# Kernel tuning notes

Measured on AMD Instinct MI355X. Metric: run time of the kernel, lower is better.

## Reference

```python
import jax, jax.numpy as jnp
import numpy as np

B, S, D, H = 4, 1024, 1024, 16
DK = D // H


def _linear_params(key, scale):
    kw, kb = jax.random.split(key)
    W = jax.random.normal(kw, (D, D), dtype=jnp.float32) * scale
    b = jax.random.normal(kb, (D,), dtype=jnp.float32) * 0.01
    return W, b


def setup_inputs() -> dict:
    key = jax.random.key(0)
    ks = jax.random.split(key, 12)
    scale = 1.0 / np.sqrt(D)
    inp = {
        "query": jax.random.normal(ks[0], (B, S, D), dtype=jnp.float32),
        "key": jax.random.normal(ks[1], (B, S, D), dtype=jnp.float32),
        "value": jax.random.normal(ks[2], (B, S, D), dtype=jnp.float32),
        "time_k": jax.random.normal(ks[3], (B, S, D), dtype=jnp.float32),
        "time_v": jax.random.normal(ks[4], (B, S, D), dtype=jnp.float32),
        "mask": jnp.zeros((B, 1, S, S), dtype=jnp.float32),
    }
    names = ["Wq", "bq", "Wk", "bk", "Wv", "bv", "Wtk", "btk", "Wtv", "btv", "Wm", "bm"]
    for i in range(6):
        W, b = _linear_params(ks[5 + i], scale)
        inp[names[2 * i]] = W
        inp[names[2 * i + 1]] = b
    return inp


def _split_heads(x):
    # [B,S,D] -> [B,H,S,DK]
    b, s, _ = x.shape
    return x.reshape(b, s, H, DK).transpose(0, 2, 1, 3)


def reference(query, key, value, time_k, time_v, mask,
              Wq, bq, Wk, bk, Wv, bv, Wtk, btk, Wtv, btv, Wm, bm):
    q = _split_heads(query @ Wq + bq)
    k = _split_heads(key @ Wk + bk)
    v = _split_heads(value @ Wv + bv)
    t_k = _split_heads(time_k @ Wtk + btk)
    t_v = _split_heads(time_v @ Wtv + btv)

    # scores[b,h,i,j] = q_i . k_j + t_k_i . q_j  (note second term uses q on the key axis)
    scores = jnp.einsum("bhid,bhjd->bhij", q, k) + jnp.einsum("bhid,bhjd->bhij", t_k, q)
    # module divides by sqrt(d_model) (query.size(-1)), not sqrt(d_k)
    scores = scores / jnp.sqrt(jnp.float32(D)) + mask
    probs = jax.nn.softmax(scores, axis=-1)

    # dropout is identity (p=0 / eval); squeeze(-2) is a no-op for S>1
    context = jnp.einsum("bhij,bhjd->bhid", probs, v) + jnp.einsum("bhij,bhjd->bhid", probs, t_v)
    x = context.transpose(0, 2, 1, 3).reshape(query.shape[0], -1, D)
    return x @ Wm + bm
```

## Files before the change

kernel.cpp:

```cpp
#include <hip/hip_runtime.h>
#include <hip/hip_bf16.h>
#include <cstdint>
#include <cstddef>

typedef __bf16 bf16;
typedef bf16 bf16x8 __attribute__((ext_vector_type(8)));
typedef bf16 bf16x4 __attribute__((ext_vector_type(4)));
typedef float f32x4 __attribute__((ext_vector_type(4)));
typedef unsigned int u32;

#define DEV static __device__ __forceinline__

DEV f32x4 mfma16(bf16x8 a, bf16x8 b, f32x4 c) {
    return __builtin_amdgcn_mfma_f32_16x16x32_bf16(a, b, c, 0, 0, 0);
}

DEV f32x4 shflx4(f32x4 v, int m) {
    f32x4 r;
    for (int i = 0; i < 4; ++i) r[i] = __shfl_xor(v[i], m, 64);
    return r;
}

DEV bf16x8 cvt8(const float* p) {
    float4 f0 = *(const float4*)p;
    float4 f1 = *(const float4*)(p + 4);
    bf16x8 v;
    v[0] = (bf16)f0.x; v[1] = (bf16)f0.y; v[2] = (bf16)f0.z; v[3] = (bf16)f0.w;
    v[4] = (bf16)f1.x; v[5] = (bf16)f1.y; v[6] = (bf16)f1.z; v[7] = (bf16)f1.w;
    return v;
}

DEV void glo(const bf16* g, bf16* l) {
    __builtin_amdgcn_global_load_lds(
        (const __attribute__((address_space(1))) u32*)g,
        (__attribute__((address_space(3))) u32*)l,
        16, 0, 0);
}

#define WAITB(n) asm volatile("s_waitcnt vmcnt(" #n ")\n\ts_barrier" ::: "memory")
#define BAR()    asm volatile("s_barrier" ::: "memory")

struct PrepArgs {
    const float* w[6];
    const float* act[5];
    const float* mask;
    bf16* wdst[6];  int wstride[6];
    bf16* adst[5];  int astride[5];
    bf16* maskR;
};

__global__ __launch_bounds__(256) void prep_kernel(PrepArgs p)
{
    const int z = blockIdx.z;
    const int t = threadIdx.x;
    if (z < 6) {
        __shared__ bf16 tile[64][72];
        const float* src = p.w[z];
        bf16* out = p.wdst[z];
        const int os = p.wstride[z];
        const int r = t >> 3, c8 = (t & 7) * 8;
        const int row0 = blockIdx.y * 64, col0 = blockIdx.x * 64;
        *(bf16x8*)&tile[r][c8]      = cvt8(&src[(size_t)(row0 + r) * 1024 + col0 + c8]);
        *(bf16x8*)&tile[r + 32][c8] = cvt8(&src[(size_t)(row0 + r + 32) * 1024 + col0 + c8]);
        __syncthreads();
        for (int half = 0; half < 2; ++half) {
            int rr = r + half * 32;
            bf16x8 v;
            for (int j = 0; j < 8; ++j) v[j] = tile[c8 + j][rr];
            *(bf16x8*)&out[(size_t)(col0 + rr) * os + row0 + c8] = v;
        }
    } else if (z < 11) {
        const float* src = p.act[z - 6];
        bf16* dst = p.adst[z - 6];
        const int as = p.astride[z - 6];
        const size_t chunk = (size_t)(blockIdx.y * 16 + blockIdx.x) * 16384;
        for (int c = 0; c < 8; ++c) {
            const size_t off = chunk + (size_t)c * 2048 + (size_t)t * 8;
            const size_t row = off >> 10, col = off & 1023;
            *(bf16x8*)&dst[row * (size_t)as + col] = cvt8(&src[off]);
        }
    } else {
        if (blockIdx.y >= 8) return;
        const int jt = blockIdx.x, it = blockIdx.y, b = z - 11;
        __shared__ bf16 Mt[128 * 72];
        const int lane = t & 63, w = t >> 6;
        const int ln = lane & 15, qd = lane >> 4;
        {
            const int il = t >> 1, jh = (t & 1) * 32;
            const float* src = &p.mask[((size_t)b * 1024 + it * 128 + il) * 1024 + jt * 64 + jh];
            *(bf16x8*)&Mt[il * 72 + jh]      = cvt8(src);
            *(bf16x8*)&Mt[il * 72 + jh + 8]  = cvt8(src + 8);
            *(bf16x8*)&Mt[il * 72 + jh + 16] = cvt8(src + 16);
            *(bf16x8*)&Mt[il * 72 + jh + 24] = cvt8(src + 24);
        }
        __syncthreads();
        bf16 m[32];
        for (int si = 0; si < 2; ++si)
            for (int jc = 0; jc < 4; ++jc)
                for (int r = 0; r < 4; ++r) {
                    const int il = w * 32 + si * 16 + qd * 4 + r;
                    const int jl = jc * 16 + ln;
                    m[(si * 4 + jc) * 4 + r] = Mt[il * 72 + jl];
                }
        bf16* dst = &p.maskR[((((size_t)b * 8 + it) * 16 + jt) * 256 + t) * 32];
        for (int c = 0; c < 4; ++c)
            *(bf16x8*)&dst[c * 8] = *(const bf16x8*)&m[c * 8];
    }
}

struct ProjArgs {
    const bf16* A[4];
    const bf16* W[4];
    const float* bias[4];
    const float* bias2[4];
    bf16* out[4];
    int vst[4];
    int nk[4];
};

__global__ __launch_bounds__(256) void proj_gemm(ProjArgs pa)
{
    const int z = blockIdx.z;
    const bf16* A = pa.A[z];
    const bf16* W = pa.W[z];
    const int nk = pa.nk[z];
    const int lda = nk << 6;
    const int m0 = blockIdx.x * 128, n0 = blockIdx.y * 128;
    __shared__ bf16 As[128 * 64];
    __shared__ bf16 Bs[128 * 64];
    const int t = threadIdx.x, lane = t & 63, w = t >> 6;
    const int ln = lane & 15, qd = lane >> 4;
    const int wm0 = (w >> 1) * 64, wn0 = (w & 1) * 64;
    const int sub0 = w * 4;
    const int rr = lane >> 3;
    const int cbs = (((lane & 7) ^ rr)) * 8;
    const int lx = ln & 7;
    f32x4 acc[4][4];
    for (int i = 0; i < 4; ++i)
        for (int j = 0; j < 4; ++j)
            acc[i][j] = (f32x4){0.f, 0.f, 0.f, 0.f};
    for (int ks = 0; ks < nk; ++ks) {
        const int bk = ks * 64;
        __syncthreads();
        for (int i = 0; i < 4; ++i) {
            const int row = (sub0 + i) * 8 + rr;
            glo(&W[(size_t)(n0 + row) * lda + bk + cbs], &Bs[(sub0 + i) * 512]);
            glo(&A[(size_t)(m0 + row) * lda + bk + cbs], &As[(sub0 + i) * 512]);
        }
        __syncthreads();
        for (int kc = 0; kc < 2; ++kc) {
            const int sg = ((kc * 4 + qd) ^ lx) * 8;
            bf16x8 af[4], bfr[4];
            for (int mi = 0; mi < 4; ++mi)
                af[mi] = *(const bf16x8*)&As[(wm0 + mi * 16 + ln) * 64 + sg];
            for (int ni = 0; ni < 4; ++ni)
                bfr[ni] = *(const bf16x8*)&Bs[(wn0 + ni * 16 + ln) * 64 + sg];
            for (int mi = 0; mi < 4; ++mi)
                for (int ni = 0; ni < 4; ++ni)
                    acc[mi][ni] = mfma16(af[mi], bfr[ni], acc[mi][ni]);
        }
    }
    const float* bias = pa.bias[z];
    const float* bias2 = pa.bias2[z];
    bf16* out = pa.out[z];
    const int vst = pa.vst[z];
    for (int ni = 0; ni < 4; ++ni) {
        const int n = n0 + wn0 + ni * 16 + ln;
        const float bv = bias[n] + (bias2 ? bias2[n] : 0.0f);
        for (int mi = 0; mi < 4; ++mi) {
            const int mbase = m0 + wm0 + mi * 16 + qd * 4;
            f32x4 v = acc[mi][ni];
            if (vst) {
                const int b = mbase >> 10, s = mbase & 1023;
                bf16x4 pk;
                for (int r = 0; r < 4; ++r) pk[r] = (bf16)(v[r] + bv);
                *(bf16x4*)&out[((size_t)(b * 1024 + n)) * 1024 + s] = pk;
            } else {
                for (int r = 0; r < 4; ++r)
                    out[(size_t)(mbase + r) * 1024 + n] = (bf16)(v[r] + bv);
            }
        }
    }
}

__global__ __launch_bounds__(256) void attn6_kernel(
    const bf16* __restrict__ Qb, const bf16* __restrict__ Kb, const bf16* __restrict__ TKb,
    const bf16* __restrict__ Vsum,
    const bf16* __restrict__ maskR, bf16* __restrict__ ctx)
{
    const int h = blockIdx.x, it = blockIdx.y, b = blockIdx.z;
    const int i0 = it * 128;
    __shared__ bf16 Ks[2][64 * 64];
    __shared__ bf16 QJs[2][64 * 64];
    __shared__ bf16 Vs[2][64 * 64];
    __shared__ bf16 Ps[128][68];
    const int t = threadIdx.x, lane = t & 63, w = t >> 6;
    const int ln = lane & 15, qd = lane >> 4;
    const int lx = ln & 7;
    const int rr = lane >> 3;
    const int cbs = ((lane & 7) ^ rr) * 8;
    const size_t baseQ = ((size_t)b * 1024) * 1024 + (size_t)h * 64;
    const size_t baseV = ((size_t)b * 1024 + h * 64) * 1024;

    bf16x8 qf[2][2], tkf[2][2];
    for (int si = 0; si < 2; ++si) {
        const size_t row = (size_t)(i0 + w * 32 + si * 16 + ln);
        for (int kc = 0; kc < 2; ++kc) {
            qf[si][kc]  = *(const bf16x8*)&Qb [baseQ + row * 1024 + kc * 32 + qd * 8];
            tkf[si][kc] = *(const bf16x8*)&TKb[baseQ + row * 1024 + kc * 32 + qd * 8];
        }
    }

    f32x4 O[2][4];
    f32x4 psum[2];
    for (int si = 0; si < 2; ++si) {
        psum[si] = (f32x4){0.f, 0.f, 0.f, 0.f};
        for (int dc = 0; dc < 4; ++dc) O[si][dc] = (f32x4){0.f, 0.f, 0.f, 0.f};
    }

    const float c1 = 0.045084439f;
    const float c2 = 1.442695041f;

    const size_t mtile0 = (((size_t)b * 8 + it) * 16) * 256 + t;

    auto stage = [&](int jt) {
        const int buf = jt & 1;
        const int j0 = jt * 64;
        for (int i = 0; i < 6; ++i) {
            const int u = w * 6 + i;
            if (u < 8) {
                glo(&Kb[baseQ + (size_t)(j0 + u * 8 + rr) * 1024 + cbs], &Ks[buf][u * 512]);
            } else if (u < 16) {
                const int s = u - 8;
                glo(&Qb[baseQ + (size_t)(j0 + s * 8 + rr) * 1024 + cbs], &QJs[buf][s * 512]);
            } else {
                const int s = u - 16;
                glo(&Vsum[baseV + (size_t)(s * 8 + rr) * 1024 + j0 + cbs], &Vs[buf][s * 512]);
            }
        }
    };

    stage(0);

    for (int jt = 0; jt < 16; ++jt) {
        const int cur = jt & 1;
        bf16x8 mm[4];
        {
            const bf16* mb = &maskR[(mtile0 + (size_t)jt * 256) * 32];
            for (int c = 0; c < 4; ++c) mm[c] = *(const bf16x8*)&mb[c * 8];
        }
        BAR();
        if (jt < 15) {
            stage(jt + 1);
            WAITB(6);
        } else {
            WAITB(0);
        }

        f32x4 sc[2][4];
        for (int jc = 0; jc < 4; ++jc) {
            bf16x8 kf[2], qjf[2];
            for (int kc = 0; kc < 2; ++kc) {
                const int sg = ((kc * 4 + qd) ^ lx) * 8;
                kf[kc]  = *(const bf16x8*)&Ks [cur][(jc * 16 + ln) * 64 + sg];
                qjf[kc] = *(const bf16x8*)&QJs[cur][(jc * 16 + ln) * 64 + sg];
            }
            for (int si = 0; si < 2; ++si) {
                f32x4 a = (f32x4){0.f, 0.f, 0.f, 0.f};
                a = mfma16(qf[si][0], kf[0], a);
                a = mfma16(qf[si][1], kf[1], a);
                a = mfma16(tkf[si][0], qjf[0], a);
                a = mfma16(tkf[si][1], qjf[1], a);
                sc[si][jc] = a;
            }
        }
        for (int si = 0; si < 2; ++si) {
            const int ibl = w * 32 + si * 16 + qd * 4;
            for (int jc = 0; jc < 4; ++jc) {
                const int jl = jc * 16 + ln;
                const int e = si * 4 + jc;
                for (int r = 0; r < 4; ++r) {
                    const float mval = (float)mm[e >> 1][(e & 1) * 4 + r];
                    const float p = exp2f(fmaf(sc[si][jc][r], c1, mval * c2));
                    psum[si][r] += p;
                    Ps[ibl + r][jl] = (bf16)p;
                }
            }
        }
        for (int kc = 0; kc < 2; ++kc) {
            bf16x8 pa[2], vb[4];
            for (int si = 0; si < 2; ++si) {
                bf16x4 lo = *(const bf16x4*)&Ps[w * 32 + si * 16 + ln][kc * 32 + qd * 8];
                bf16x4 hi = *(const bf16x4*)&Ps[w * 32 + si * 16 + ln][kc * 32 + qd * 8 + 4];
                for (int e = 0; e < 4; ++e) { pa[si][e] = lo[e]; pa[si][4 + e] = hi[e]; }
            }
            for (int dc = 0; dc < 4; ++dc) {
                const int vrow = dc * 16 + ln;
                const int sg = ((kc * 4 + qd) ^ lx) * 8;
                vb[dc] = *(const bf16x8*)&Vs[cur][vrow * 64 + sg];
            }
            for (int si = 0; si < 2; ++si)
                for (int dc = 0; dc < 4; ++dc)
                    O[si][dc] = mfma16(pa[si], vb[dc], O[si][dc]);
        }
    }

    for (int si = 0; si < 2; ++si) {
        for (int m = 1; m <= 8; m <<= 1) psum[si] += shflx4(psum[si], m);
        f32x4 rl;
        for (int r = 0; r < 4; ++r) rl[r] = 1.0f / psum[si][r];
        const int ibase = i0 + w * 32 + si * 16 + qd * 4;
        for (int dc = 0; dc < 4; ++dc) {
            const int d = h * 64 + dc * 16 + ln;
            f32x4 v = O[si][dc] * rl;
            for (int r = 0; r < 4; ++r)
                ctx[((size_t)b * 1024 + ibase + r) * 1024 + d] = (bf16)v[r];
        }
    }
}

__global__ __launch_bounds__(256) void out_gemm(
    const bf16* __restrict__ A, const bf16* __restrict__ W,
    const float* __restrict__ bias, float* __restrict__ out)
{
    const int m0 = blockIdx.x * 64, n0 = blockIdx.y * 128;
    __shared__ bf16 As[2][64 * 64];
    __shared__ bf16 Bs[2][128 * 64];
    const int t = threadIdx.x, lane = t & 63, w = t >> 6;
    const int ln = lane & 15, qd = lane >> 4;
    const int wn0 = w * 32;
    const int rr = lane >> 3;
    const int cbs = ((lane & 7) ^ rr) * 8;
    const int lx = ln & 7;
    f32x4 acc[4][2];
    for (int i = 0; i < 4; ++i)
        for (int j = 0; j < 2; ++j)
            acc[i][j] = (f32x4){0.f, 0.f, 0.f, 0.f};

    auto stage = [&](int ks) {
        const int buf = ks & 1;
        const int bk = ks * 64;
        for (int i = 0; i < 6; ++i) {
            const int u = w * 6 + i;
            if (u < 8) {
                glo(&A[(size_t)(m0 + u * 8 + rr) * 1024 + bk + cbs], &As[buf][u * 512]);
            } else {
                const int sub = u - 8;
                glo(&W[(size_t)(n0 + sub * 8 + rr) * 1024 + bk + cbs], &Bs[buf][sub * 512]);
            }
        }
    };

    stage(0);

    for (int ks = 0; ks < 16; ++ks) {
        const int cur = ks & 1;
        BAR();
        if (ks < 15) {
            stage(ks + 1);
            WAITB(6);
        } else {
            WAITB(0);
        }
        for (int kc = 0; kc < 2; ++kc) {
            const int sg = ((kc * 4 + qd) ^ lx) * 8;
            bf16x8 af[4], bfr[2];
            for (int mi = 0; mi < 4; ++mi)
                af[mi] = *(const bf16x8*)&As[cur][(mi * 16 + ln) * 64 + sg];
            for (int ni = 0; ni < 2; ++ni)
                bfr[ni] = *(const bf16x8*)&Bs[cur][(wn0 + ni * 16 + ln) * 64 + sg];
            for (int mi = 0; mi < 4; ++mi)
                for (int ni = 0; ni < 2; ++ni)
                    acc[mi][ni] = mfma16(af[mi], bfr[ni], acc[mi][ni]);
        }
    }
    for (int ni = 0; ni < 2; ++ni) {
        const int n = n0 + wn0 + ni * 16 + ln;
        const float bv = bias[n];
        for (int mi = 0; mi < 4; ++mi) {
            const int mbase = m0 + mi * 16 + qd * 4;
            f32x4 v = acc[mi][ni];
            for (int r = 0; r < 4; ++r)
                out[(size_t)(mbase + r) * 1024 + n] = v[r] + bv;
        }
    }
}

extern "C" void kernel_launch(void* const* d_in, const int* in_sizes, int n_in,
                              void* d_out, int out_size, void* d_ws, size_t ws_size,
                              hipStream_t stream)
{
    (void)in_sizes; (void)n_in; (void)out_size; (void)ws_size;
    const float* query  = (const float*)d_in[0];
    const float* key    = (const float*)d_in[1];
    const float* value  = (const float*)d_in[2];
    const float* time_k = (const float*)d_in[3];
    const float* time_v = (const float*)d_in[4];
    const float* mask   = (const float*)d_in[5];
    const float* Wq  = (const float*)d_in[6];  const float* bq  = (const float*)d_in[7];
    const float* Wk  = (const float*)d_in[8];  const float* bk  = (const float*)d_in[9];
    const float* Wv  = (const float*)d_in[10]; const float* bv  = (const float*)d_in[11];
    const float* Wtk = (const float*)d_in[12]; const float* btk = (const float*)d_in[13];
    const float* Wtv = (const float*)d_in[14]; const float* btv = (const float*)d_in[15];
    const float* Wm  = (const float*)d_in[16]; const float* bm  = (const float*)d_in[17];

    bf16* ws = (bf16*)d_ws;
    const size_t MM = (size_t)1024 * 1024;
    bf16* WTq  = ws + 0 * MM;
    bf16* WTk  = ws + 1 * MM;
    bf16* WTtk = ws + 2 * MM;
    bf16* WTm  = ws + 3 * MM;
    bf16* WT5  = ws + 4 * MM;
    bf16* qbf  = ws + 6 * MM;
    bf16* kbf  = ws + 10 * MM;
    bf16* tkbf = ws + 14 * MM;
    bf16* A5   = ws + 18 * MM;
    bf16* Qb   = ws + 26 * MM;
    bf16* Kb   = ws + 30 * MM;
    bf16* TKb  = ws + 34 * MM;
    bf16* VsT  = ws + 38 * MM;
    bf16* ctx  = ws + 6 * MM;
    bf16* maskR = (bf16*)d_out;

    PrepArgs pp;
    pp.w[0] = Wq;  pp.wdst[0] = WTq;        pp.wstride[0] = 1024;
    pp.w[1] = Wk;  pp.wdst[1] = WTk;        pp.wstride[1] = 1024;
    pp.w[2] = Wv;  pp.wdst[2] = WT5;        pp.wstride[2] = 2048;
    pp.w[3] = Wtk; pp.wdst[3] = WTtk;       pp.wstride[3] = 1024;
    pp.w[4] = Wtv; pp.wdst[4] = WT5 + 1024; pp.wstride[4] = 2048;
    pp.w[5] = Wm;  pp.wdst[5] = WTm;        pp.wstride[5] = 1024;
    pp.act[0] = query;  pp.adst[0] = qbf;       pp.astride[0] = 1024;
    pp.act[1] = key;    pp.adst[1] = kbf;       pp.astride[1] = 1024;
    pp.act[2] = value;  pp.adst[2] = A5;        pp.astride[2] = 2048;
    pp.act[3] = time_k; pp.adst[3] = tkbf;      pp.astride[3] = 1024;
    pp.act[4] = time_v; pp.adst[4] = A5 + 1024; pp.astride[4] = 2048;
    pp.mask = mask; pp.maskR = maskR;
    prep_kernel<<<dim3(16, 16, 15), 256, 0, stream>>>(pp);

    ProjArgs pa;
    pa.A[0] = qbf;  pa.W[0] = WTq;  pa.bias[0] = bq;  pa.bias2[0] = nullptr;
    pa.out[0] = Qb;  pa.vst[0] = 0; pa.nk[0] = 16;
    pa.A[1] = kbf;  pa.W[1] = WTk;  pa.bias[1] = bk;  pa.bias2[1] = nullptr;
    pa.out[1] = Kb;  pa.vst[1] = 0; pa.nk[1] = 16;
    pa.A[2] = tkbf; pa.W[2] = WTtk; pa.bias[2] = btk; pa.bias2[2] = nullptr;
    pa.out[2] = TKb; pa.vst[2] = 0; pa.nk[2] = 16;
    pa.A[3] = A5;   pa.W[3] = WT5;  pa.bias[3] = bv;  pa.bias2[3] = btv;
    pa.out[3] = VsT; pa.vst[3] = 1; pa.nk[3] = 32;
    proj_gemm<<<dim3(32, 8, 4), 256, 0, stream>>>(pa);

    attn6_kernel<<<dim3(16, 8, 4), 256, 0, stream>>>(
        Qb, Kb, TKb, VsT, maskR, ctx);
    out_gemm<<<dim3(64, 8), 256, 0, stream>>>(ctx, WTm, bm, (float*)d_out);
}
```

Baseline: 315.5 us.

## Fuse fp32-to-bf16 activation conversion into projection GEMM A-tile loads

Drops the activation-conversion part of the prep kernel. The projection GEMM now reads fp32 activations directly, converts them to bf16 in registers and stores them into LDS, with the next k-step's A tile prefetched into registers during compute. This removes a full write and re-read of five bf16 activation copies, roughly 100MB of extra traffic. In exchange the A-operand path uses register loads instead of async global_load_lds, which adds register pressure and VALU conversion work inside the GEMM. A launch-bounds occupancy hint is also added.

New measurement: 373.6 us. +18.4%, slower.

```diff
diff --git a/kernel.cpp b/kernel.cpp
--- a/kernel.cpp
+++ b/kernel.cpp
@@ -42,10 +42,8 @@
 
 struct PrepArgs {
     const float* w[6];
-    const float* act[5];
     const float* mask;
     bf16* wdst[6];  int wstride[6];
-    bf16* adst[5];  int astride[5];
     bf16* maskR;
 };
 
@@ -69,19 +67,9 @@
             for (int j = 0; j < 8; ++j) v[j] = tile[c8 + j][rr];
             *(bf16x8*)&out[(size_t)(col0 + rr) * os + row0 + c8] = v;
         }
-    } else if (z < 11) {
-        const float* src = p.act[z - 6];
-        bf16* dst = p.adst[z - 6];
-        const int as = p.astride[z - 6];
-        const size_t chunk = (size_t)(blockIdx.y * 16 + blockIdx.x) * 16384;
-        for (int c = 0; c < 8; ++c) {
-            const size_t off = chunk + (size_t)c * 2048 + (size_t)t * 8;
-            const size_t row = off >> 10, col = off & 1023;
-            *(bf16x8*)&dst[row * (size_t)as + col] = cvt8(&src[off]);
-        }
     } else {
         if (blockIdx.y >= 8) return;
-        const int jt = blockIdx.x, it = blockIdx.y, b = z - 11;
+        const int jt = blockIdx.x, it = blockIdx.y, b = z - 6;
         __shared__ bf16 Mt[128 * 72];
         const int lane = t & 63, w = t >> 6;
         const int ln = lane & 15, qd = lane >> 4;
@@ -109,7 +97,8 @@
 }
 
 struct ProjArgs {
-    const bf16* A[4];
+    const float* A0[4];
+    const float* A1[4];
     const bf16* W[4];
     const float* bias[4];
     const float* bias2[4];
@@ -118,11 +107,12 @@
     int nk[4];
 };
 
-__global__ __launch_bounds__(256) void proj_gemm(ProjArgs pa)
+__global__ __launch_bounds__(256, 4) void proj_gemm(ProjArgs pa)
 {
     const int z = blockIdx.z;
-    const bf16* A = pa.A[z];
-    const bf16* W = pa.W[z];
+    const float* __restrict__ A0 = pa.A0[z];
+    const float* __restrict__ A1 = pa.A1[z];
+    const bf16* __restrict__ W = pa.W[z];
     const int nk = pa.nk[z];
     const int lda = nk << 6;
     const int m0 = blockIdx.x * 128, n0 = blockIdx.y * 128;
@@ -139,15 +129,30 @@
     for (int i = 0; i < 4; ++i)
         for (int j = 0; j < 4; ++j)
             acc[i][j] = (f32x4){0.f, 0.f, 0.f, 0.f};
+
+    bf16x8 av[4];
+    auto loadA = [&](int ks) {
+        const int bk = ks * 64;
+        const float* src = (bk < 1024) ? A0 : A1;
+        const int acol = (bk & 1023) + cbs;
+        for (int i = 0; i < 4; ++i) {
+            const int row = (sub0 + i) * 8 + rr;
+            av[i] = cvt8(&src[(size_t)(m0 + row) * 1024 + acol]);
+        }
+    };
+
+    loadA(0);
     for (int ks = 0; ks < nk; ++ks) {
         const int bk = ks * 64;
         __syncthreads();
         for (int i = 0; i < 4; ++i) {
             const int row = (sub0 + i) * 8 + rr;
             glo(&W[(size_t)(n0 + row) * lda + bk + cbs], &Bs[(sub0 + i) * 512]);
-            glo(&A[(size_t)(m0 + row) * lda + bk + cbs], &As[(sub0 + i) * 512]);
-        }
+        }
+        for (int i = 0; i < 4; ++i)
+            *(bf16x8*)&As[(sub0 + i) * 512 + lane * 8] = av[i];
         __syncthreads();
+        if (ks + 1 < nk) loadA(ks + 1);
         for (int kc = 0; kc < 2; ++kc) {
             const int sg = ((kc * 4 + qd) ^ lx) * 8;
             bf16x8 af[4], bfr[4];
@@ -411,15 +416,11 @@
     bf16* WTtk = ws + 2 * MM;
     bf16* WTm  = ws + 3 * MM;
     bf16* WT5  = ws + 4 * MM;
-    bf16* qbf  = ws + 6 * MM;
-    bf16* kbf  = ws + 10 * MM;
-    bf16* tkbf = ws + 14 * MM;
-    bf16* A5   = ws + 18 * MM;
-    bf16* Qb   = ws + 26 * MM;
-    bf16* Kb   = ws + 30 * MM;
-    bf16* TKb  = ws + 34 * MM;
-    bf16* VsT  = ws + 38 * MM;
-    bf16* ctx  = ws + 6 * MM;
+    bf16* Qb   = ws + 6 * MM;
+    bf16* Kb   = ws + 10 * MM;
+    bf16* TKb  = ws + 14 * MM;
+    bf16* VsT  = ws + 18 * MM;
+    bf16* ctx  = ws + 22 * MM;
     bf16* maskR = (bf16*)d_out;
 
     PrepArgs pp;
@@ -429,22 +430,17 @@
     pp.w[3] = Wtk; pp.wdst[3] = WTtk;       pp.wstride[3] = 1024;
     pp.w[4] = Wtv; pp.wdst[4] = WT5 + 1024; pp.wstride[4] = 2048;
     pp.w[5] = Wm;  pp.wdst[5] = WTm;        pp.wstride[5] = 1024;
-    pp.act[0] = query;  pp.adst[0] = qbf;       pp.astride[0] = 1024;
-    pp.act[1] = key;    pp.adst[1] = kbf;       pp.astride[1] = 1024;
-    pp.act[2] = value;  pp.adst[2] = A5;        pp.astride[2] = 2048;
-    pp.act[3] = time_k; pp.adst[3] = tkbf;      pp.astride[3] = 1024;
-    pp.act[4] = time_v; pp.adst[4] = A5 + 1024; pp.astride[4] = 2048;
     pp.mask = mask; pp.maskR = maskR;
-    prep_kernel<<<dim3(16, 16, 15), 256, 0, stream>>>(pp);
+    prep_kernel<<<dim3(16, 16, 10), 256, 0, stream>>>(pp);
 
     ProjArgs pa;
-    pa.A[0] = qbf;  pa.W[0] = WTq;  pa.bias[0] = bq;  pa.bias2[0] = nullptr;
+    pa.A0[0] = query;  pa.A1[0] = nullptr; pa.W[0] = WTq;  pa.bias[0] = bq;  pa.bias2[0] = nullptr;
     pa.out[0] = Qb;  pa.vst[0] = 0; pa.nk[0] = 16;
-    pa.A[1] = kbf;  pa.W[1] = WTk;  pa.bias[1] = bk;  pa.bias2[1] = nullptr;
+    pa.A0[1] = key;    pa.A1[1] = nullptr; pa.W[1] = WTk;  pa.bias[1] = bk;  pa.bias2[1] = nullptr;
     pa.out[1] = Kb;  pa.vst[1] = 0; pa.nk[1] = 16;
-    pa.A[2] = tkbf; pa.W[2] = WTtk; pa.bias[2] = btk; pa.bias2[2] = nullptr;
+    pa.A0[2] = time_k; pa.A1[2] = nullptr; pa.W[2] = WTtk; pa.bias[2] = btk; pa.bias2[2] = nullptr;
     pa.out[2] = TKb; pa.vst[2] = 0; pa.nk[2] = 16;
-    pa.A[3] = A5;   pa.W[3] = WT5;  pa.bias[3] = bv;  pa.bias2[3] = btv;
+    pa.A0[3] = value;  pa.A1[3] = time_v;  pa.W[3] = WT5;  pa.bias[3] = bv;  pa.bias2[3] = btv;
     pa.out[3] = VsT; pa.vst[3] = 1; pa.nk[3] = 32;
     proj_gemm<<<dim3(32, 8, 4), 256, 0, stream>>>(pa);
 
```

## Enlarge projection GEMM tiles to 256x256 with double-buffered interleaved prefetch

Applied to the files above, without the earlier changes.

The projection GEMM now uses 512-thread blocks computing 256x256 tiles, with double-buffered LDS. Global-to-LDS loads for the next K step are split across four compute phases, so they overlap MFMA work, and s_setprio raises priority around the MFMA bursts. The long-K fused V/time_v projection moves to z=0 so it is scheduled first. This removes the per-step sync stall of the old load-then-compute loop and raises operand reuse. In exchange it cuts the grid to 256 blocks and uses 128KB of LDS per block, which lowers occupancy and may leave some CUs idle.

Result: slower. 327.3 us (+3.7%).

```diff
diff --git a/kernel.cpp b/kernel.cpp
--- a/kernel.cpp
+++ b/kernel.cpp
@@ -118,48 +118,101 @@
     int nk[4];
 };
 
-__global__ __launch_bounds__(256) void proj_gemm(ProjArgs pa)
+__global__ __launch_bounds__(512, 2) void proj_gemm(ProjArgs pa)
 {
     const int z = blockIdx.z;
-    const bf16* A = pa.A[z];
-    const bf16* W = pa.W[z];
+    const bf16* __restrict__ A = pa.A[z];
+    const bf16* __restrict__ W = pa.W[z];
     const int nk = pa.nk[z];
     const int lda = nk << 6;
-    const int m0 = blockIdx.x * 128, n0 = blockIdx.y * 128;
-    __shared__ bf16 As[128 * 64];
-    __shared__ bf16 Bs[128 * 64];
+    const int m0 = blockIdx.x * 256, n0 = blockIdx.y * 256;
+    __shared__ bf16 As[2][256 * 64];
+    __shared__ bf16 Bs[2][256 * 64];
     const int t = threadIdx.x, lane = t & 63, w = t >> 6;
     const int ln = lane & 15, qd = lane >> 4;
-    const int wm0 = (w >> 1) * 64, wn0 = (w & 1) * 64;
-    const int sub0 = w * 4;
+    const int wm0 = (w >> 2) * 128, wn0 = (w & 3) * 64;
     const int rr = lane >> 3;
-    const int cbs = (((lane & 7) ^ rr)) * 8;
+    const int cbs = ((lane & 7) ^ rr) * 8;
     const int lx = ln & 7;
-    f32x4 acc[4][4];
-    for (int i = 0; i < 4; ++i)
+    const int u0 = w * 4;
+
+    f32x4 acc[8][4];
+    for (int i = 0; i < 8; ++i)
         for (int j = 0; j < 4; ++j)
             acc[i][j] = (f32x4){0.f, 0.f, 0.f, 0.f};
+
+#define SA(ks_, i_, b_) glo(&A[(size_t)(m0 + (u0 + (i_)) * 8 + rr) * lda + (ks_) * 64 + cbs], \
+                            &As[b_][(u0 + (i_)) * 512])
+#define SB(ks_, i_, b_) glo(&W[(size_t)(n0 + (u0 + (i_)) * 8 + rr) * lda + (ks_) * 64 + cbs], \
+                            &Bs[b_][(u0 + (i_)) * 512])
+
+    SA(0, 0, 0); SA(0, 1, 0); SA(0, 2, 0); SA(0, 3, 0);
+    SB(0, 0, 0); SB(0, 1, 0); SB(0, 2, 0); SB(0, 3, 0);
+    WAITB(0);
+
     for (int ks = 0; ks < nk; ++ks) {
-        const int bk = ks * 64;
-        __syncthreads();
-        for (int i = 0; i < 4; ++i) {
-            const int row = (sub0 + i) * 8 + rr;
-            glo(&W[(size_t)(n0 + row) * lda + bk + cbs], &Bs[(sub0 + i) * 512]);
-            glo(&A[(size_t)(m0 + row) * lda + bk + cbs], &As[(sub0 + i) * 512]);
-        }
-        __syncthreads();
-        for (int kc = 0; kc < 2; ++kc) {
-            const int sg = ((kc * 4 + qd) ^ lx) * 8;
-            bf16x8 af[4], bfr[4];
-            for (int mi = 0; mi < 4; ++mi)
-                af[mi] = *(const bf16x8*)&As[(wm0 + mi * 16 + ln) * 64 + sg];
+        const int cur = ks & 1, nxt = cur ^ 1;
+        const bool pf = (ks + 1 < nk);
+        bf16x8 af[4], bfr[4];
+        {
+            const int sg = (qd ^ lx) * 8;
             for (int ni = 0; ni < 4; ++ni)
-                bfr[ni] = *(const bf16x8*)&Bs[(wn0 + ni * 16 + ln) * 64 + sg];
+                bfr[ni] = *(const bf16x8*)&Bs[cur][(wn0 + ni * 16 + ln) * 64 + sg];
+            for (int mi = 0; mi < 4; ++mi)
+                af[mi] = *(const bf16x8*)&As[cur][(wm0 + mi * 16 + ln) * 64 + sg];
+            if (pf) { SA(ks + 1, 0, nxt); SA(ks + 1, 1, nxt); SA(ks + 1, 2, nxt); }
+            BAR();
+            __builtin_amdgcn_s_setprio(1);
             for (int mi = 0; mi < 4; ++mi)
                 for (int ni = 0; ni < 4; ++ni)
                     acc[mi][ni] = mfma16(af[mi], bfr[ni], acc[mi][ni]);
-        }
-    }
+            __builtin_amdgcn_s_setprio(0);
+            BAR();
+        }
+        {
+            const int sg = (qd ^ lx) * 8;
+            for (int mi = 0; mi < 4; ++mi)
+                af[mi] = *(const bf16x8*)&As[cur][(wm0 + 64 + mi * 16 + ln) * 64 + sg];
+            if (pf) { SA(ks + 1, 3, nxt); SB(ks + 1, 0, nxt); SB(ks + 1, 1, nxt); }
+            BAR();
+            __builtin_amdgcn_s_setprio(1);
+            for (int mi = 0; mi < 4; ++mi)
+                for (int ni = 0; ni < 4; ++ni)
+                    acc[4 + mi][ni] = mfma16(af[mi], bfr[ni], acc[4 + mi][ni]);
+            __builtin_amdgcn_s_setprio(0);
+            BAR();
+        }
+        {
+            const int sg = ((4 + qd) ^ lx) * 8;
+            for (int ni = 0; ni < 4; ++ni)
+                bfr[ni] = *(const bf16x8*)&Bs[cur][(wn0 + ni * 16 + ln) * 64 + sg];
+            for (int mi = 0; mi < 4; ++mi)
+                af[mi] = *(const bf16x8*)&As[cur][(wm0 + mi * 16 + ln) * 64 + sg];
+            if (pf) { SB(ks + 1, 2, nxt); SB(ks + 1, 3, nxt); }
+            BAR();
+            __builtin_amdgcn_s_setprio(1);
+            for (int mi = 0; mi < 4; ++mi)
+                for (int ni = 0; ni < 4; ++ni)
+                    acc[mi][ni] = mfma16(af[mi], bfr[ni], acc[mi][ni]);
+            __builtin_amdgcn_s_setprio(0);
+            BAR();
+        }
+        {
+            const int sg = ((4 + qd) ^ lx) * 8;
+            for (int mi = 0; mi < 4; ++mi)
+                af[mi] = *(const bf16x8*)&As[cur][(wm0 + 64 + mi * 16 + ln) * 64 + sg];
+            BAR();
+            __builtin_amdgcn_s_setprio(1);
+            for (int mi = 0; mi < 4; ++mi)
+                for (int ni = 0; ni < 4; ++ni)
+                    acc[4 + mi][ni] = mfma16(af[mi], bfr[ni], acc[4 + mi][ni]);
+            __builtin_amdgcn_s_setprio(0);
+            WAITB(0);
+        }
+    }
+#undef SA
+#undef SB
+
     const float* bias = pa.bias[z];
     const float* bias2 = pa.bias2[z];
     bf16* out = pa.out[z];
@@ -167,7 +220,7 @@
     for (int ni = 0; ni < 4; ++ni) {
         const int n = n0 + wn0 + ni * 16 + ln;
         const float bv = bias[n] + (bias2 ? bias2[n] : 0.0f);
-        for (int mi = 0; mi < 4; ++mi) {
+        for (int mi = 0; mi < 8; ++mi) {
             const int mbase = m0 + wm0 + mi * 16 + qd * 4;
             f32x4 v = acc[mi][ni];
             if (vst) {
@@ -438,15 +491,15 @@
     prep_kernel<<<dim3(16, 16, 15), 256, 0, stream>>>(pp);
 
     ProjArgs pa;
-    pa.A[0] = qbf;  pa.W[0] = WTq;  pa.bias[0] = bq;  pa.bias2[0] = nullptr;
-    pa.out[0] = Qb;  pa.vst[0] = 0; pa.nk[0] = 16;
-    pa.A[1] = kbf;  pa.W[1] = WTk;  pa.bias[1] = bk;  pa.bias2[1] = nullptr;
-    pa.out[1] = Kb;  pa.vst[1] = 0; pa.nk[1] = 16;
-    pa.A[2] = tkbf; pa.W[2] = WTtk; pa.bias[2] = btk; pa.bias2[2] = nullptr;
-    pa.out[2] = TKb; pa.vst[2] = 0; pa.nk[2] = 16;
-    pa.A[3] = A5;   pa.W[3] = WT5;  pa.bias[3] = bv;  pa.bias2[3] = btv;
-    pa.out[3] = VsT; pa.vst[3] = 1; pa.nk[3] = 32;
-    proj_gemm<<<dim3(32, 8, 4), 256, 0, stream>>>(pa);
+    pa.A[0] = A5;   pa.W[0] = WT5;  pa.bias[0] = bv;  pa.bias2[0] = btv;
+    pa.out[0] = VsT; pa.vst[0] = 1; pa.nk[0] = 32;
+    pa.A[1] = qbf;  pa.W[1] = WTq;  pa.bias[1] = bq;  pa.bias2[1] = nullptr;
+    pa.out[1] = Qb;  pa.vst[1] = 0; pa.nk[1] = 16;
+    pa.A[2] = kbf;  pa.W[2] = WTk;  pa.bias[2] = bk;  pa.bias2[2] = nullptr;
+    pa.out[2] = Kb;  pa.vst[2] = 0; pa.nk[2] = 16;
+    pa.A[3] = tkbf; pa.W[3] = WTtk; pa.bias[3] = btk; pa.bias2[3] = nullptr;
+    pa.out[3] = TKb; pa.vst[3] = 0; pa.nk[3] = 16;
+    proj_gemm<<<dim3(16, 4, 4), 512, 0, stream>>>(pa);
 
     attn6_kernel<<<dim3(16, 8, 4), 256, 0, stream>>>(
         Qb, Kb, TKb, VsT, maskR, ctx);
```
